# Performance work log

Measured on AMD Instinct MI355X. Metric: run time of the kernel, lower is better.

The kernel has to match this reference:

```python
import jax, jax.numpy as jnp
import numpy as np

N_ENT = 50000     # n_entities
C = 128           # channel
N_EDGES = 1600000 # n_edges (avg degree 32)
N_REL = 11        # n_relations; edge_type in [1, N_REL-1]
N_HOPS = 3
EPS = 1e-12       # F.normalize default eps


def setup_inputs() -> dict:
    key = jax.random.key(0)
    k1, k2, k3, k4 = jax.random.split(key, 4)
    entity_emb = jax.random.normal(k1, (N_ENT, C), dtype=jnp.float32)
    edge_index = jax.random.randint(k2, (2, N_EDGES), 0, N_ENT, dtype=jnp.int64)
    edge_type = jax.random.randint(k3, (N_EDGES,), 1, N_REL, dtype=jnp.int64)
    # xavier_uniform bound for (N_REL-1, C)
    bound = float(np.sqrt(6.0 / ((N_REL - 1) + C)))
    weight = jax.random.uniform(k4, (N_REL - 1, C), jnp.float32, -bound, bound)
    return {"entity_emb": entity_emb, "edge_index": edge_index,
            "edge_type": edge_type, "weight": weight}


def reference(entity_emb, edge_index, edge_type, weight):
    head, tail = edge_index[0], edge_index[1]
    # relation embedding per edge: weight[edge_type - 1] -> [E, C]
    rel_emb = weight[edge_type - 1]
    ones = jnp.ones((edge_index.shape[1],), entity_emb.dtype)
    # per-head in-degree counts (constant across hops)
    cnt = jax.ops.segment_sum(ones, head, num_segments=N_ENT)
    denom = jnp.maximum(cnt, 1.0)[:, None]  # scatter_mean: zero rows stay zero

    def hop(emb):
        msg = emb[tail] * rel_emb                                   # gather + mul [E, C]
        agg = jax.ops.segment_sum(msg, head, num_segments=N_ENT) / denom  # scatter_mean
        # F.normalize (L2 per row)
        norm = jnp.linalg.norm(agg, axis=1, keepdims=True)
        return agg / jnp.maximum(norm, EPS)

    res = entity_emb
    emb = entity_emb
    for _ in range(N_HOPS):
        emb = hop(emb)
        res = res + emb
    return res
```

## Files before the change

kernel.cpp:

```cpp
#include <hip/hip_runtime.h>

#define N_ENT   50000
#define CH      128
#define N_EDGES 1600000
#define N_RELM1 10
#define NB      391
#define BCAP    4608
#define PART_BLOCKS 512
#define CHUNK   (N_EDGES / PART_BLOCKS)
#define EPS_N   1e-12f

__device__ __forceinline__ unsigned int f2bf_bits(float f) {
    unsigned int x = __float_as_uint(f);
    return (x + 0x7FFFu + ((x >> 16) & 1u)) >> 16;
}

__global__ __launch_bounds__(256) void gc_part_kernel(const int* __restrict__ head,
                                                      const int* __restrict__ tail,
                                                      const int* __restrict__ etyp,
                                                      int* __restrict__ barr,
                                                      int* __restrict__ cnts,
                                                      int* __restrict__ boffs,
                                                      const float* __restrict__ ent,
                                                      unsigned int* __restrict__ emb) {
    __shared__ int hist[512];
    __shared__ int fctr[512];
    __shared__ int boff_s[512];
    __shared__ int psum[256];
    __shared__ int stage[CHUNK];
    int tid = threadIdx.x, blk = blockIdx.x;
    for (int i = tid; i < 512; i += 256) { hist[i] = 0; fctr[i] = 0; }
    __syncthreads();
    int lo = blk * CHUNK;
    for (int e = lo + tid; e < lo + CHUNK; e += 256)
        atomicAdd(&hist[head[e] >> 7], 1);
    __syncthreads();
    int a0 = hist[2 * tid], a1 = hist[2 * tid + 1];
    int s2 = a0 + a1;
    psum[tid] = s2;
    __syncthreads();
    for (int d = 1; d < 256; d <<= 1) {
        int t = (tid >= d) ? psum[tid - d] : 0;
        __syncthreads();
        psum[tid] += t;
        __syncthreads();
    }
    int excl = psum[tid] - s2;
    boff_s[2 * tid] = excl;
    boff_s[2 * tid + 1] = excl + a0;
    __syncthreads();
    for (int e = lo + tid; e < lo + CHUNK; e += 256) {
        int h = head[e];
        int b = h >> 7;
        int pos = boff_s[b] + atomicAdd(&fctr[b], 1);
        stage[pos] = (tail[e] & 0xFFFF) | ((etyp[e] - 1) << 16) | ((h & 127) << 20);
    }
    __syncthreads();
    for (int i = tid; i < CHUNK; i += 256) barr[lo + i] = stage[i];
    for (int i = tid; i < NB; i += 256) {
        cnts[blk * NB + i] = fctr[i];
        boffs[blk * NB + i] = boff_s[i];
    }
    for (int i = blk * 256 + tid; i < N_ENT * (CH / 2); i += PART_BLOCKS * 256) {
        float2 v = *(const float2*)(ent + 2 * (size_t)i);
        emb[i] = f2bf_bits(v.x) | (f2bf_bits(v.y) << 16);
    }
}

__global__ __launch_bounds__(512) void gc_place_kernel(const int* __restrict__ barr,
                                                       const int* __restrict__ cnts,
                                                       const int* __restrict__ boffs,
                                                       unsigned int* __restrict__ off_deg,
                                                       int* __restrict__ csr) {
    __shared__ int ent_s[BCAP];
    __shared__ int psum[512];
    __shared__ int hcnt[128];
    __shared__ int hloc[128];
    __shared__ int hctr[128];
    int b = blockIdx.x, tid = threadIdx.x;
    if (tid < 128) { hcnt[tid] = 0; hctr[tid] = 0; }
    int c = cnts[tid * NB + b];
    int o = boffs[tid * NB + b];
    psum[tid] = c;
    __syncthreads();
    for (int d = 1; d < 512; d <<= 1) {
        int t = (tid >= d) ? psum[tid - d] : 0;
        __syncthreads();
        psum[tid] += t;
        __syncthreads();
    }
    int my_off = psum[tid] - c;
    int n = psum[511];
    const int* src = barr + tid * CHUNK + o;
    for (int k = 0; k < c; ++k) ent_s[my_off + k] = src[k];
    __syncthreads();
    for (int i = tid; i < n; i += 512)
        atomicAdd(&hcnt[(ent_s[i] >> 20) & 127], 1);
    __syncthreads();
    int v = (tid < 128) ? hcnt[tid] : 0;
    for (int d = 1; d < 128; d <<= 1) {
        int t = (tid < 128 && tid >= d) ? hcnt[tid - d] : 0;
        __syncthreads();
        if (tid < 128) hcnt[tid] += t;
        __syncthreads();
    }
    int lo = b * BCAP;
    if (tid < 128) {
        int start = lo + hcnt[tid] - v;
        hloc[tid] = start;
        int h = (b << 7) + tid;
        if (h < N_ENT) off_deg[h] = ((unsigned)start << 11) | (unsigned)v;
    }
    __syncthreads();
    for (int i = tid; i < n; i += 512) {
        int e = ent_s[i];
        int hl = (e >> 20) & 127;
        int pos = hloc[hl] + atomicAdd(&hctr[hl], 1);
        csr[pos] = e & 0xFFFFF;
    }
}

__global__ __launch_bounds__(256) void gc_hop_kernel(
        const unsigned int* __restrict__ src,
        const unsigned int* __restrict__ off_deg,
        const int* __restrict__ csr,
        const float* __restrict__ wt,
        unsigned int* __restrict__ dst,
        float* __restrict__ res,
        const float* __restrict__ ent,
        int init) {
    __shared__ float wt_s[N_RELM1 * CH];
    for (int i = threadIdx.x; i < N_RELM1 * CH; i += 256) wt_s[i] = wt[i];
    __syncthreads();

    int wave = threadIdx.x >> 6, lane = threadIdx.x & 63;
    int row = __builtin_amdgcn_readfirstlane(blockIdx.x * 4 + wave);

    unsigned od = (unsigned)__builtin_amdgcn_readfirstlane((int)off_deg[row]);
    int seg = (int)(od >> 11);
    int deg = (int)(od & 2047u);
    int seg_end = seg + deg;

    float ax = 0.f, ay = 0.f;
    int j = seg;
    for (; j + 8 <= seg_end; j += 8) {
        int pk[8];
        #pragma unroll
        for (int u = 0; u < 8; ++u)
            pk[u] = __builtin_amdgcn_readfirstlane(csr[j + u]);
        #pragma unroll
        for (int u = 0; u < 8; ++u) {
            unsigned v = src[pk[u] % 65536 * 64 + lane];
            float2 w = *(const float2*)(&wt_s[(pk[u] >> 16) * CH + 2 * lane]);
            ax = fmaf(__uint_as_float(v << 16), w.x, ax);
            ay = fmaf(__uint_as_float(v & 0xFFFF0000u), w.y, ay);
        }
    }
    for (; j < seg_end; ++j) {
        int pk = __builtin_amdgcn_readfirstlane(csr[j]);
        unsigned v = src[pk % 65536 * 64 + lane];
        float2 w = *(const float2*)(&wt_s[(pk >> 16) * CH + 2 * lane]);
        ax = fmaf(__uint_as_float(v << 16), w.x, ax);
        ay = fmaf(__uint_as_float(v & 0xFFFF0000u), w.y, ay);
    }

    float invd = 1.0f / fmaxf((float)deg, 1.0f);
    float x0 = ax * invd, x1 = ay * invd;

    float s = x0 * x0 + x1 * x1;
    #pragma unroll
    for (int o = 32; o > 0; o >>= 1) s += __shfl_down(s, o, 64);
    s = __shfl(s, 0, 64);

    float inv = 1.0f / fmaxf(sqrtf(s), EPS_N);
    float y0 = x0 * inv, y1 = x1 * inv;

    dst[(row << 6) + lane] = f2bf_bits(y0) | (f2bf_bits(y1) << 16);

    int base = (row << 7) + 2 * lane;
    if (init) {
        float2 e = *(const float2*)(ent + base);
        *(float2*)(res + base) = make_float2(e.x + y0, e.y + y1);
    } else {
        float2 rv = *(const float2*)(res + base);
        *(float2*)(res + base) = make_float2(rv.x + y0, rv.y + y1);
    }
}

extern "C" void kernel_launch(void* const* d_in, const int* in_sizes, int n_in,
                              void* d_out, int out_size, void* d_ws, size_t ws_size,
                              hipStream_t stream) {
    const float* ent  = (const float*)d_in[0];
    const int*   eidx = (const int*)d_in[1];
    const int*   etyp = (const int*)d_in[2];
    const float* wt   = (const float*)d_in[3];
    float*       res  = (float*)d_out;

    const int* head = eidx;
    const int* tail = eidx + N_EDGES;

    unsigned int* embA = (unsigned int*)d_ws;
    unsigned int* embB = embA + (size_t)N_ENT * 64;
    int* barr  = (int*)(embB + (size_t)N_ENT * 64);
    int* cnts  = barr + N_EDGES;
    int* boffs = cnts + PART_BLOCKS * NB;
    unsigned int* off_deg = (unsigned int*)(boffs + PART_BLOCKS * NB);
    int* csr   = (int*)(off_deg + N_ENT);

    gc_part_kernel<<<PART_BLOCKS, 256, 0, stream>>>(head, tail, etyp, barr, cnts,
                                                    boffs, ent, embA);
    gc_place_kernel<<<NB, 512, 0, stream>>>(barr, cnts, boffs, off_deg, csr);

    const int hop_grid = N_ENT / 4;
    gc_hop_kernel<<<hop_grid, 256, 0, stream>>>(embA, off_deg, csr, wt, embB, res, ent, 1);
    gc_hop_kernel<<<hop_grid, 256, 0, stream>>>(embB, off_deg, csr, wt, embA, res, ent, 0);
    gc_hop_kernel<<<hop_grid, 256, 0, stream>>>(embA, off_deg, csr, wt, embB, res, ent, 0);
}
```

Before: 303.2 us.

## Stage edges in LDS during partition, pack bucket counts/offsets, widen place kernel

The partition kernel now reads head/tail/type from global memory once, keeps the packed edge and its bucket id in shared memory, and reuses them for the scatter pass instead of re-reading global memory. Per-bucket count and offset are packed into one int, halving that metadata traffic. Partition blocks go from 512 to 800, and the place kernel uses 1024 threads to cover them. The packing assumes each block's per-bucket count fits in 8 bits, and the larger shared-memory footprint may lower occupancy.

```diff
diff --git a/kernel.cpp b/kernel.cpp
--- a/kernel.cpp
+++ b/kernel.cpp
@@ -6,7 +6,7 @@
 #define N_RELM1 10
 #define NB      391
 #define BCAP    4608
-#define PART_BLOCKS 512
+#define PART_BLOCKS 800
 #define CHUNK   (N_EDGES / PART_BLOCKS)
 #define EPS_N   1e-12f
 
@@ -19,21 +19,28 @@
                                                       const int* __restrict__ tail,
                                                       const int* __restrict__ etyp,
                                                       int* __restrict__ barr,
-                                                      int* __restrict__ cnts,
-                                                      int* __restrict__ boffs,
+                                                      int* __restrict__ pack,
                                                       const float* __restrict__ ent,
                                                       unsigned int* __restrict__ emb) {
     __shared__ int hist[512];
+    __shared__ int boff_s[512];
     __shared__ int fctr[512];
-    __shared__ int boff_s[512];
     __shared__ int psum[256];
-    __shared__ int stage[CHUNK];
+    __shared__ int stageE[CHUNK];
+    __shared__ unsigned short stageB[CHUNK];
+    __shared__ int stage2[CHUNK];
     int tid = threadIdx.x, blk = blockIdx.x;
     for (int i = tid; i < 512; i += 256) { hist[i] = 0; fctr[i] = 0; }
     __syncthreads();
     int lo = blk * CHUNK;
-    for (int e = lo + tid; e < lo + CHUNK; e += 256)
-        atomicAdd(&hist[head[e] >> 7], 1);
+    for (int i = tid; i < CHUNK; i += 256) {
+        int e = lo + i;
+        int h = head[e];
+        int b = h >> 7;
+        stageE[i] = (tail[e] & 0xFFFF) | ((etyp[e] - 1) << 16) | ((h & 127) << 20);
+        stageB[i] = (unsigned short)b;
+        atomicAdd(&hist[b], 1);
+    }
     __syncthreads();
     int a0 = hist[2 * tid], a1 = hist[2 * tid + 1];
     int s2 = a0 + a1;
@@ -49,52 +56,52 @@
     boff_s[2 * tid] = excl;
     boff_s[2 * tid + 1] = excl + a0;
     __syncthreads();
-    for (int e = lo + tid; e < lo + CHUNK; e += 256) {
-        int h = head[e];
-        int b = h >> 7;
+    for (int i = tid; i < CHUNK; i += 256) {
+        int b = stageB[i];
         int pos = boff_s[b] + atomicAdd(&fctr[b], 1);
-        stage[pos] = (tail[e] & 0xFFFF) | ((etyp[e] - 1) << 16) | ((h & 127) << 20);
-    }
-    __syncthreads();
-    for (int i = tid; i < CHUNK; i += 256) barr[lo + i] = stage[i];
-    for (int i = tid; i < NB; i += 256) {
-        cnts[blk * NB + i] = fctr[i];
-        boffs[blk * NB + i] = boff_s[i];
-    }
+        stage2[pos] = stageE[i];
+    }
+    __syncthreads();
+    for (int i = tid; i < CHUNK; i += 256) barr[lo + i] = stage2[i];
+    for (int i = tid; i < NB; i += 256)
+        pack[blk * NB + i] = (boff_s[i] << 8) | fctr[i];
     for (int i = blk * 256 + tid; i < N_ENT * (CH / 2); i += PART_BLOCKS * 256) {
         float2 v = *(const float2*)(ent + 2 * (size_t)i);
         emb[i] = f2bf_bits(v.x) | (f2bf_bits(v.y) << 16);
     }
 }
 
-__global__ __launch_bounds__(512) void gc_place_kernel(const int* __restrict__ barr,
-                                                       const int* __restrict__ cnts,
-                                                       const int* __restrict__ boffs,
-                                                       unsigned int* __restrict__ off_deg,
-                                                       int* __restrict__ csr) {
+__global__ __launch_bounds__(1024) void gc_place_kernel(const int* __restrict__ barr,
+                                                        const int* __restrict__ pack,
+                                                        unsigned int* __restrict__ off_deg,
+                                                        int* __restrict__ csr) {
     __shared__ int ent_s[BCAP];
-    __shared__ int psum[512];
+    __shared__ int psum[1024];
     __shared__ int hcnt[128];
     __shared__ int hloc[128];
     __shared__ int hctr[128];
     int b = blockIdx.x, tid = threadIdx.x;
     if (tid < 128) { hcnt[tid] = 0; hctr[tid] = 0; }
-    int c = cnts[tid * NB + b];
-    int o = boffs[tid * NB + b];
+    int c = 0, o = 0;
+    if (tid < PART_BLOCKS) {
+        int pk = pack[tid * NB + b];
+        c = pk & 255;
+        o = pk >> 8;
+    }
     psum[tid] = c;
     __syncthreads();
-    for (int d = 1; d < 512; d <<= 1) {
+    for (int d = 1; d < 1024; d <<= 1) {
         int t = (tid >= d) ? psum[tid - d] : 0;
         __syncthreads();
         psum[tid] += t;
         __syncthreads();
     }
     int my_off = psum[tid] - c;
-    int n = psum[511];
+    int n = psum[1023];
     const int* src = barr + tid * CHUNK + o;
     for (int k = 0; k < c; ++k) ent_s[my_off + k] = src[k];
     __syncthreads();
-    for (int i = tid; i < n; i += 512)
+    for (int i = tid; i < n; i += 1024)
         atomicAdd(&hcnt[(ent_s[i] >> 20) & 127], 1);
     __syncthreads();
     int v = (tid < 128) ? hcnt[tid] : 0;
@@ -112,7 +119,7 @@
         if (h < N_ENT) off_deg[h] = ((unsigned)start << 11) | (unsigned)v;
     }
     __syncthreads();
-    for (int i = tid; i < n; i += 512) {
+    for (int i = tid; i < n; i += 1024) {
         int e = ent_s[i];
         int hl = (e >> 20) & 127;
         int pos = hloc[hl] + atomicAdd(&hctr[hl], 1);
@@ -202,14 +209,13 @@
     unsigned int* embA = (unsigned int*)d_ws;
     unsigned int* embB = embA + (size_t)N_ENT * 64;
     int* barr  = (int*)(embB + (size_t)N_ENT * 64);
-    int* cnts  = barr + N_EDGES;
-    int* boffs = cnts + PART_BLOCKS * NB;
-    unsigned int* off_deg = (unsigned int*)(boffs + PART_BLOCKS * NB);
+    int* pack  = barr + N_EDGES;
+    unsigned int* off_deg = (unsigned int*)(pack + PART_BLOCKS * NB);
     int* csr   = (int*)(off_deg + N_ENT);
 
-    gc_part_kernel<<<PART_BLOCKS, 256, 0, stream>>>(head, tail, etyp, barr, cnts,
-                                                    boffs, ent, embA);
-    gc_place_kernel<<<NB, 512, 0, stream>>>(barr, cnts, boffs, off_deg, csr);
+    gc_part_kernel<<<PART_BLOCKS, 256, 0, stream>>>(head, tail, etyp, barr, pack,
+                                                    ent, embA);
+    gc_place_kernel<<<NB, 1024, 0, stream>>>(barr, pack, off_deg, csr);
 
     const int hop_grid = N_ENT / 4;
     gc_hop_kernel<<<hop_grid, 256, 0, stream>>>(embA, off_deg, csr, wt, embB, res, ent, 1);
```

Measured after the change: 298.3 us. Within noise of the previous version (-1.6%).
